# Performance work log

Measured on AMD Instinct MI355X. Metric: run time of the kernel, lower is better.

## Reference

```python
import jax, jax.numpy as jnp
import numpy as np
import math

B, N, C, A, H = 1, 320, 128, 32, 4  # batch, n_res, rep_2d channels, attn channels, heads


def _layernorm(x, w, b, eps=1e-5):
    mu = jnp.mean(x, axis=-1, keepdims=True)
    var = jnp.var(x, axis=-1, keepdims=True)
    return (x - mu) * jax.lax.rsqrt(var + eps) * w + b


def setup_inputs() -> dict:
    key = jax.random.key(0)
    ks = jax.random.split(key, 12)
    s = 0.02
    return {
        "x2d": jax.random.normal(ks[0], (B, N, N, C), dtype=jnp.float32),
        "mask": jnp.ones((B, N, N), dtype=jnp.float32),
        "norm_w": jnp.ones((C,), dtype=jnp.float32),
        "norm_b": jnp.zeros((C,), dtype=jnp.float32),
        "Wq": jax.random.normal(ks[1], (C, A * H), dtype=jnp.float32) * s,
        "Wk": jax.random.normal(ks[2], (C, A * H), dtype=jnp.float32) * s,
        "Wv": jax.random.normal(ks[3], (C, A * H), dtype=jnp.float32) * s,
        "Wb": jax.random.normal(ks[4], (C, H), dtype=jnp.float32) * s,
        "Wg": jax.random.normal(ks[5], (C, A * H), dtype=jnp.float32) * s,
        "bg": jnp.zeros((A * H,), dtype=jnp.float32),
        "Wo": jax.random.normal(ks[6], (A * H, C), dtype=jnp.float32) * s,
        "bo": jnp.zeros((C,), dtype=jnp.float32),
    }


def reference(x2d, mask, norm_w, norm_b, Wq, Wk, Wv, Wb, Wg, bg, Wo, bo):
    xn = _layernorm(x2d, norm_w, norm_b)                      # [B,N,N,C]
    # note: torch .view(..., A, H) splits the output channel as (A, H)
    q = (xn @ Wq).reshape(B, N, N, A, H)
    k = (xn @ Wk).reshape(B, N, N, A, H)
    v = (xn @ Wv).reshape(B, N, N, A, H)
    b = xn @ Wb                                               # [B,N,N,H] -> b[b,j,k,h]
    g = jax.nn.sigmoid((xn @ Wg + bg).reshape(B, N, N, A, H))
    w = jnp.einsum('bijch,bikch->bijkh', q, k) / math.sqrt(A)
    # torch: b.unsqueeze(1).transpose(2,3) => w[b,i,j,k,h] += b[b,k,j,h]
    w = w + jnp.transpose(b, (0, 2, 1, 3))[:, None]           # [B,1,N,N,H]
    w = (w + 100.0) * mask[:, :, None, :, None] - 100.0
    w = jax.nn.softmax(w, axis=-2)                            # over k
    out = jnp.einsum('bijkh,bikch->bijch', w, v) * g          # [B,N,N,A,H]
    out = out.reshape(B, N, N, A * H) @ Wo + bo               # [B,N,N,C]
    out = out * mask[..., None]
    return out
```

## Files before the change

### kernel.cpp

```cpp
#include <hip/hip_runtime.h>
#include <hip/hip_bf16.h>
#include <math.h>

#define N 320
#define C 128
#define A 32
#define H 4
#define NPOS (N*N)

typedef __attribute__((ext_vector_type(8))) __bf16 bf16x8;
typedef __attribute__((ext_vector_type(16))) float f32x16;

union frag_u { int4 i; bf16x8 v; unsigned u[4]; };

#define MFMA32(va, vb, vc) __builtin_amdgcn_mfma_f32_32x32x16_bf16((va), (vb), (vc), 0, 0, 0)

#define WAVE_LDS_FENCE() do { \
    asm volatile("s_waitcnt lgkmcnt(0)" ::: "memory"); \
    __builtin_amdgcn_sched_barrier(0); \
} while (0)

static __device__ __forceinline__ unsigned pk_bf16(float lo, float hi) {
    union { __hip_bfloat162 h; unsigned u; } cv;
    cv.h = __float22bfloat162_rn(make_float2(lo, hi));
    return cv.u;
}

static __device__ __forceinline__ float bf16_to_f32(unsigned short u) {
    union { unsigned u; float f; } c;
    c.u = ((unsigned)u) << 16;
    return c.f;
}

__global__ __launch_bounds__(256)
void wprep_kernel(const float* __restrict__ Wq,
                  const float* __restrict__ Wk,
                  const float* __restrict__ Wv,
                  const float* __restrict__ Wg,
                  const float* __restrict__ Wo,
                  unsigned short* __restrict__ WF) {
    const float isq = 0.17677669529663687f;
    int tid = blockIdx.x * 256 + threadIdx.x;
    int lane = tid & 63;
    int kk = (tid >> 6) & 7;
    int ct = (tid >> 9) & 3;
    int mat = tid >> 11;
    const float* src = (mat == 0) ? Wq : (mat == 1) ? Wk : (mat == 2) ? Wv
                     : (mat == 3) ? Wg : Wo;
    float scl = (mat == 0) ? isq : 1.0f;
    int col = ct * 32 + (lane & 31);
    int c0 = kk * 16 + (lane >> 5) * 8;
    float v[8];
    #pragma unroll
    for (int e = 0; e < 8; e++) {
        int rr = c0 + e;
        int srow = (mat == 4) ? (((rr & 31) << 2) | (rr >> 5)) : rr;
        v[e] = src[(size_t)srow * 128 + col] * scl;
    }
    int4 out;
    out.x = pk_bf16(v[0], v[1]);
    out.y = pk_bf16(v[2], v[3]);
    out.z = pk_bf16(v[4], v[5]);
    out.w = pk_bf16(v[6], v[7]);
    *(int4*)((char*)WF + (size_t)tid * 16) = out;
}

__global__ __launch_bounds__(256)
void btrans_kernel(const float* __restrict__ Bp, float* __restrict__ BpT) {
    __shared__ float tile[64][65];
    const int b = blockIdx.x;
    const int h = b / 25;
    const int bk = (b % 25) / 5;
    const int bj = b % 5;
    const int k0 = bk * 64, j0 = bj * 64;
    const float* src = Bp + (size_t)h * NPOS;
    float* dst = BpT + (size_t)h * NPOS;
    const int t = threadIdx.x;
    #pragma unroll
    for (int u = 0; u < 16; ++u) {
        int idx = u * 256 + t;
        int kk = idx >> 6, jj = idx & 63;
        tile[kk][jj] = src[(size_t)(k0 + kk) * N + j0 + jj];
    }
    __syncthreads();
    #pragma unroll
    for (int u = 0; u < 16; ++u) {
        int idx = u * 256 + t;
        int jj = idx >> 6, kk = idx & 63;
        dst[(size_t)(j0 + jj) * N + k0 + kk] = tile[kk][jj];
    }
}

__global__ __launch_bounds__(256)
void ln_proj_kernel(const float* __restrict__ x2d,
                    const float* __restrict__ norm_w,
                    const float* __restrict__ norm_b,
                    const float* __restrict__ Wb,
                    const float* __restrict__ bg,
                    const unsigned short* __restrict__ WF,
                    unsigned short* __restrict__ Qb,
                    unsigned short* __restrict__ Kb,
                    unsigned short* __restrict__ Vta,
                    unsigned short* __restrict__ Gb,
                    float* __restrict__ Bp) {
    __shared__ __align__(16) unsigned char shbuf[16896];
    unsigned char* xnb = shbuf;

    const int t = threadIdx.x;
    const int gpos0 = blockIdx.x * 32;

    {
        const int r = t >> 3, s = t & 7;
        const float4* src = (const float4*)(x2d + (size_t)(gpos0 + r) * 128 + s * 16);
        float4 xv[4];
        #pragma unroll
        for (int u = 0; u < 4; u++) xv[u] = src[u];
        float sum = 0.f, sq = 0.f;
        #pragma unroll
        for (int u = 0; u < 4; u++) {
            sum += xv[u].x + xv[u].y + xv[u].z + xv[u].w;
            sq += xv[u].x * xv[u].x + xv[u].y * xv[u].y
                + xv[u].z * xv[u].z + xv[u].w * xv[u].w;
        }
        sum += __shfl_xor(sum, 1); sum += __shfl_xor(sum, 2); sum += __shfl_xor(sum, 4);
        sq  += __shfl_xor(sq, 1);  sq  += __shfl_xor(sq, 2);  sq  += __shfl_xor(sq, 4);
        float mean = sum * (1.0f / 128.0f);
        float var  = sq * (1.0f / 128.0f) - mean * mean;
        float rstd = rsqrtf(var + 1e-5f);

        const float4* wsrc = (const float4*)(norm_w + s * 16);
        const float4* bsrc = (const float4*)(norm_b + s * 16);
        const float4* wb4  = (const float4*)Wb;
        float pb0 = 0.f, pb1 = 0.f, pb2 = 0.f, pb3 = 0.f;
        float4 xe;
        #pragma unroll
        for (int u = 0; u < 4; u++) {
            float4 wv = wsrc[u], bv = bsrc[u], x4 = xv[u];
            float4 xn;
            xn.x = (x4.x - mean) * rstd * wv.x + bv.x;
            xn.y = (x4.y - mean) * rstd * wv.y + bv.y;
            xn.z = (x4.z - mean) * rstd * wv.z + bv.z;
            xn.w = (x4.w - mean) * rstd * wv.w + bv.w;
            int cb = s * 16 + u * 4;
            float4 w0 = wb4[cb + 0], w1 = wb4[cb + 1], w2 = wb4[cb + 2], w3 = wb4[cb + 3];
            pb0 = fmaf(xn.x, w0.x, fmaf(xn.y, w1.x, fmaf(xn.z, w2.x, fmaf(xn.w, w3.x, pb0))));
            pb1 = fmaf(xn.x, w0.y, fmaf(xn.y, w1.y, fmaf(xn.z, w2.y, fmaf(xn.w, w3.y, pb1))));
            pb2 = fmaf(xn.x, w0.z, fmaf(xn.y, w1.z, fmaf(xn.z, w2.z, fmaf(xn.w, w3.z, pb2))));
            pb3 = fmaf(xn.x, w0.w, fmaf(xn.y, w1.w, fmaf(xn.z, w2.w, fmaf(xn.w, w3.w, pb3))));
            if (u & 1) {
                int g = s * 2 + (u >> 1);
                int4 gr;
                gr.x = pk_bf16(xe.x, xe.y);
                gr.y = pk_bf16(xe.z, xe.w);
                gr.z = pk_bf16(xn.x, xn.y);
                gr.w = pk_bf16(xn.z, xn.w);
                *(int4*)(xnb + r * 256 + ((g ^ (r & 7)) << 4)) = gr;
            } else {
                xe = xn;
            }
        }
        pb0 += __shfl_xor(pb0, 1); pb0 += __shfl_xor(pb0, 2); pb0 += __shfl_xor(pb0, 4);
        pb1 += __shfl_xor(pb1, 1); pb1 += __shfl_xor(pb1, 2); pb1 += __shfl_xor(pb1, 4);
        pb2 += __shfl_xor(pb2, 1); pb2 += __shfl_xor(pb2, 2); pb2 += __shfl_xor(pb2, 4);
        pb3 += __shfl_xor(pb3, 1); pb3 += __shfl_xor(pb3, 2); pb3 += __shfl_xor(pb3, 4);
        if (s < 4) {
            float pbsel = (s == 0) ? pb0 : (s == 1) ? pb1 : (s == 2) ? pb2 : pb3;
            Bp[(size_t)s * NPOS + gpos0 + r] = pbsel;
        }
    }
    __syncthreads();

    const int lane = t & 63;
    const int w = t >> 6;
    const int col = lane & 31;
    const int hi = lane >> 5;

    frag_u af[8];
    #pragma unroll
    for (int kk = 0; kk < 8; kk++)
        af[kk].i = *(const int4*)(xnb + col * 256 + (((kk * 2 + hi) ^ (col & 7)) << 4));
    __syncthreads();

    const char* wf = (const char*)WF + (size_t)w * 4 * 8 * 1024;
    float* stage_w = (float*)shbuf + w * 1056;

    for (int ct = 0; ct < 4; ct++) {
        f32x16 acc;
        #pragma unroll
        for (int r = 0; r < 16; r++) acc[r] = 0.f;
        #pragma unroll
        for (int kk = 0; kk < 8; kk++) {
            frag_u bf;
            bf.i = *(const int4*)(wf + (ct * 8 + kk) * 1024 + lane * 16);
            acc = MFMA32(af[kk].v, bf.v, acc);
        }
        #pragma unroll
        for (int r = 0; r < 16; r++) {
            int patr = (r & 3) + 8 * (r >> 2) + 4 * hi;
            stage_w[col * 33 + patr] = acc[r];
        }
        WAVE_LDS_FENCE();
        if (w < 2) {
            char* dst = (w == 0) ? (char*)Qb : (char*)Kb;
            #pragma unroll
            for (int h = 0; h < 4; h++) {
                float f[4];
                #pragma unroll
                for (int e = 0; e < 4; e++)
                    f[e] = stage_w[((hi * 4 + e) * 4 + h) * 33 + col];
                uint2 val;
                val.x = pk_bf16(f[0], f[1]);
                val.y = pk_bf16(f[2], f[3]);
                *(uint2*)(dst + ((size_t)(h * 4 + ct) * NPOS + gpos0 + col) * 16 + hi * 8) = val;
            }
        } else if (w == 2) {
            int cc = col, half = hi;
            int plane = (cc & 3) * 32 + ct * 8 + (cc >> 2);
            unsigned pk[8];
            #pragma unroll
            for (int j2 = 0; j2 < 8; j2++)
                pk[j2] = pk_bf16(stage_w[cc * 33 + half * 16 + 2 * j2],
                                 stage_w[cc * 33 + half * 16 + 2 * j2 + 1]);
            int4* dst = (int4*)((char*)Vta + ((size_t)plane * NPOS + gpos0 + half * 16) * 2);
            dst[0] = make_int4(pk[0], pk[1], pk[2], pk[3]);
            dst[1] = make_int4(pk[4], pk[5], pk[6], pk[7]);
        } else {
            #pragma unroll
            for (int h = 0; h < 4; h++) {
                float f[4];
                #pragma unroll
                for (int e = 0; e < 4; e++) {
                    float z = stage_w[((hi * 4 + e) * 4 + h) * 33 + col]
                            + bg[ct * 32 + (hi * 4 + e) * 4 + h];
                    f[e] = 1.0f / (1.0f + __expf(-z));
                }
                uint2 val;
                val.x = pk_bf16(f[0], f[1]);
                val.y = pk_bf16(f[2], f[3]);
                *(uint2*)((char*)Gb + ((size_t)(h * 4 + ct) * NPOS + gpos0 + col) * 16 + hi * 8) = val;
            }
        }
        WAVE_LDS_FENCE();
    }
}

__global__ __launch_bounds__(320, 2)
void attn_kernel(const unsigned short* __restrict__ Qb,
                 const unsigned short* __restrict__ Kb,
                 const unsigned short* __restrict__ Vta,
                 const unsigned short* __restrict__ Gb,
                 const float* __restrict__ BpT,
                 const float* __restrict__ mask,
                 unsigned short* __restrict__ Ob) {
    __shared__ __align__(16) unsigned char smem[40960];
    __shared__ float mparr[320];
    __shared__ float m2arr[320];
    unsigned char* Klds = smem;
    unsigned char* Vlds = smem + 20480;

    const int i = blockIdx.x >> 2;
    const int h = blockIdx.x & 3;
    const int t = threadIdx.x;
    const int lane = t & 63;
    const int w = t >> 6;
    const int col = lane & 31;
    const int hi = lane >> 5;
    const int jt0 = w * 64;

    frag_u qf[2][2];
    const char* qplane = (const char*)Qb + ((size_t)(h * 4) * NPOS + (size_t)i * N) * 16;
    #pragma unroll
    for (int jt = 0; jt < 2; ++jt) {
        int jrow = jt0 + jt * 32 + col;
        #pragma unroll
        for (int cf = 0; cf < 2; ++cf) {
            int g = cf * 2 + hi;
            qf[jt][cf].i = *(const int4*)(qplane + ((size_t)g * NPOS + jrow) * 16);
        }
    }

    const char* kplane = (const char*)Kb + ((size_t)(h * 4) * NPOS + (size_t)i * N) * 16;
    #pragma unroll
    for (int it = 0; it < 4; ++it) {
        int4 val = *(const int4*)(kplane + ((size_t)it * NPOS + t) * 16);
        *(int4*)(Klds + t * 64 + ((it ^ ((t >> 1) & 3)) << 4)) = val;
    }
    const char* vbsrc = (const char*)Vta + ((size_t)h * 32 * NPOS + (size_t)i * N) * 2;
    #pragma unroll
    for (int it = 0; it < 4; ++it) {
        int tt = t + it * 320;
        int a = tt / 40, kg = tt % 40;
        int4 val = *(const int4*)(vbsrc + (size_t)a * NPOS * 2 + kg * 16);
        *(int4*)(Vlds + a * 640 + ((kg ^ (a & 7)) << 4)) = val;
    }
    {
        int kt_ = t >> 5, hi_ = (t >> 4) & 1, r_ = t & 15;
        int k = kt_ * 32 + (r_ & 3) + 8 * (r_ >> 2) + 4 * hi_;
        float m_ = mask[(size_t)i * N + k];
        mparr[t] = m_;
        m2arr[t] = fmaf(100.f, m_, -100.f);
    }
    __syncthreads();

    f32x16 accO[2];
    #pragma unroll
    for (int r = 0; r < 16; ++r) { accO[0][r] = 0.f; accO[1][r] = 0.f; }
    float lsum[2] = { 0.f, 0.f };

    const float* br0 = BpT + (size_t)h * NPOS + (size_t)(jt0 + col) * N + 4 * hi;
    const float* br1 = br0 + (size_t)32 * N;

    float4 b0[4], b1[4];
    #pragma unroll
    for (int q = 0; q < 4; ++q) b0[q] = *(const float4*)(br0 + 8 * q);

#define PROCESS_JT(JT, BB)                                                      \
    {                                                                           \
        f32x16 S;                                                               \
        _Pragma("unroll") for (int r = 0; r < 16; ++r) S[r] = 0.f;              \
        __builtin_amdgcn_s_setprio(1);                                          \
        S = MFMA32(kf0.v, qf[JT][0].v, S);                                      \
        S = MFMA32(kf1.v, qf[JT][1].v, S);                                      \
        __builtin_amdgcn_s_setprio(0);                                          \
        float pe[16];                                                           \
        float l0 = 0.f, l1 = 0.f, l2 = 0.f, l3 = 0.f;                           \
        _Pragma("unroll") for (int q = 0; q < 4; ++q) {                         \
            float sv0 = fmaf(S[4*q+0] + BB[q].x, mk4[q].x, m2v[q].x);           \
            float sv1 = fmaf(S[4*q+1] + BB[q].y, mk4[q].y, m2v[q].y);           \
            float sv2 = fmaf(S[4*q+2] + BB[q].z, mk4[q].z, m2v[q].z);           \
            float sv3 = fmaf(S[4*q+3] + BB[q].w, mk4[q].w, m2v[q].w);           \
            pe[4*q+0] = __expf(sv0); pe[4*q+1] = __expf(sv1);                   \
            pe[4*q+2] = __expf(sv2); pe[4*q+3] = __expf(sv3);                   \
            l0 += pe[4*q+0]; l1 += pe[4*q+1];                                   \
            l2 += pe[4*q+2]; l3 += pe[4*q+3];                                   \
        }                                                                       \
        lsum[JT] += (l0 + l1) + (l2 + l3);                                      \
        unsigned p[8];                                                          \
        _Pragma("unroll") for (int q = 0; q < 8; ++q)                           \
            p[q] = pk_bf16(pe[2 * q], pe[2 * q + 1]);                           \
        unsigned x0 = p[0], y0 = p[2];                                          \
        unsigned x1 = p[1], y1 = p[3];                                          \
        unsigned x2 = p[4], y2 = p[6];                                          \
        unsigned x3 = p[5], y3 = p[7];                                          \
        asm("v_permlane32_swap_b32 %0, %1" : "+v"(x0), "+v"(y0));               \
        asm("v_permlane32_swap_b32 %0, %1" : "+v"(x1), "+v"(y1));               \
        asm("v_permlane32_swap_b32 %0, %1" : "+v"(x2), "+v"(y2));               \
        asm("v_permlane32_swap_b32 %0, %1" : "+v"(x3), "+v"(y3));               \
        frag_u bf0, bf1;                                                        \
        bf0.u[0] = x0; bf0.u[1] = x1; bf0.u[2] = y0; bf0.u[3] = y1;             \
        bf1.u[0] = x2; bf1.u[1] = x3; bf1.u[2] = y2; bf1.u[3] = y3;             \
        __builtin_amdgcn_s_setprio(1);                                          \
        accO[JT] = MFMA32(vf0.v, bf0.v, accO[JT]);                              \
        accO[JT] = MFMA32(vf1.v, bf1.v, accO[JT]);                              \
        __builtin_amdgcn_s_setprio(0);                                          \
    }

    for (int kt = 0; kt < 10; ++kt) {
        const int kbase = kt * 32;
        const int krow = kbase + col;
        frag_u kf0, kf1, vf0, vf1;
        kf0.i = *(const int4*)(Klds + krow * 64 + (((0 + hi) ^ ((krow >> 1) & 3)) << 4));
        kf1.i = *(const int4*)(Klds + krow * 64 + (((2 + hi) ^ ((krow >> 1) & 3)) << 4));
        vf0.i = *(const int4*)(Vlds + col * 640 + (((kt * 4 + 0 + hi) ^ (col & 7)) << 4));
        vf1.i = *(const int4*)(Vlds + col * 640 + (((kt * 4 + 2 + hi) ^ (col & 7)) << 4));

        float4 mk4[4], m2v[4];
        const float* mp  = mparr + kbase + hi * 16;
        const float* m2p = m2arr + kbase + hi * 16;
        #pragma unroll
        for (int q = 0; q < 4; ++q) {
            mk4[q] = *(const float4*)(mp + 4 * q);
            m2v[q] = *(const float4*)(m2p + 4 * q);
        }

        #pragma unroll
        for (int q = 0; q < 4; ++q) b1[q] = *(const float4*)(br1 + kbase + 8 * q);

        PROCESS_JT(0, b0)

        if (kt < 9) {
            #pragma unroll
            for (int q = 0; q < 4; ++q) b0[q] = *(const float4*)(br0 + kbase + 32 + 8 * q);
        }

        PROCESS_JT(1, b1)
    }
#undef PROCESS_JT

    __syncthreads();
    float* st = (float*)(smem + w * 8192);
    const char* gplane = (const char*)Gb + ((size_t)(h * 4) * NPOS + (size_t)i * N) * 16;

    #pragma unroll
    for (int jt = 0; jt < 2; ++jt) {
        float lt = lsum[jt] + __shfl_xor(lsum[jt], 32);
        float inv = 1.0f / lt;
        #pragma unroll
        for (int r = 0; r < 16; ++r) {
            const int a = (r & 3) + 8 * (r >> 2) + 4 * hi;
            st[col * 33 + a] = accO[jt][r] * inv;
        }
        WAVE_LDS_FENCE();
        {
            int jj = lane & 31;
            int ah0 = hi * 16;
            int jrow = jt0 + jt * 32 + jj;
            int4 g0 = *(const int4*)(gplane + ((size_t)(2 * hi + 0) * NPOS + jrow) * 16);
            int4 g1 = *(const int4*)(gplane + ((size_t)(2 * hi + 1) * NPOS + jrow) * 16);
            unsigned gw[8] = { (unsigned)g0.x, (unsigned)g0.y, (unsigned)g0.z, (unsigned)g0.w,
                               (unsigned)g1.x, (unsigned)g1.y, (unsigned)g1.z, (unsigned)g1.w };
            unsigned pk8[8];
            #pragma unroll
            for (int e = 0; e < 8; ++e) {
                float ge0 = bf16_to_f32((unsigned short)(gw[e] & 0xffffu));
                float ge1 = bf16_to_f32((unsigned short)(gw[e] >> 16));
                pk8[e] = pk_bf16(st[jj * 33 + ah0 + 2 * e + 0] * ge0,
                                 st[jj * 33 + ah0 + 2 * e + 1] * ge1);
            }
            char* dst = (char*)Ob + (((size_t)i * N + jrow) * 128 + h * 32 + ah0) * 2;
            *(int4*)dst = make_int4(pk8[0], pk8[1], pk8[2], pk8[3]);
            *(int4*)(dst + 16) = make_int4(pk8[4], pk8[5], pk8[6], pk8[7]);
        }
        WAVE_LDS_FENCE();
    }
}

__global__ __launch_bounds__(256)
void outproj_kernel(const unsigned short* __restrict__ Ob,
                    const unsigned short* __restrict__ WoF,
                    const float* __restrict__ bo,
                    const float* __restrict__ mask,
                    float* __restrict__ out) {
    __shared__ __align__(16) unsigned char obs[64 * 256];
    __shared__ float stage[4][32 * 65];

    const int t = threadIdx.x;
    const int gpos0 = blockIdx.x * 64;

    {
        const int r = t >> 2, s = t & 3;
        const char* src = (const char*)Ob + ((size_t)(gpos0 + r) * 128 + s * 32) * 2;
        #pragma unroll
        for (int u = 0; u < 4; ++u) {
            int4 v = *(const int4*)(src + u * 16);
            int g = s * 4 + u;
            *(int4*)(obs + r * 256 + ((g ^ (r & 7)) << 4)) = v;
        }
    }
    __syncthreads();

    const int lane = t & 63;
    const int w = t >> 6;
    const int col = lane & 31;
    const int hi = lane >> 5;

    f32x16 acc0, acc1;
    float bocol = bo[w * 32 + col];
    #pragma unroll
    for (int r = 0; r < 16; ++r) { acc0[r] = bocol; acc1[r] = bocol; }

    const char* wf = (const char*)WoF + (size_t)w * 8 * 1024;
    #pragma unroll
    for (int kk = 0; kk < 8; ++kk) {
        frag_u bf, a0, a1;
        bf.i = *(const int4*)(wf + kk * 1024 + lane * 16);
        int row0 = col, row1 = 32 + col;
        a0.i = *(const int4*)(obs + row0 * 256 + (((kk * 2 + hi) ^ (row0 & 7)) << 4));
        a1.i = *(const int4*)(obs + row1 * 256 + (((kk * 2 + hi) ^ (row1 & 7)) << 4));
        acc0 = MFMA32(a0.v, bf.v, acc0);
        acc1 = MFMA32(a1.v, bf.v, acc1);
    }

    float* st = stage[w];
    #pragma unroll
    for (int r = 0; r < 16; ++r) {
        int patr = (r & 3) + 8 * (r >> 2) + 4 * hi;
        st[col * 65 + patr] = acc0[r];
        st[col * 65 + 32 + patr] = acc1[r];
    }
    WAVE_LDS_FENCE();
    {
        int row = lane;
        float mv = mask[gpos0 + row];
        float4* dst = (float4*)(out + (size_t)(gpos0 + row) * 128 + w * 32);
        #pragma unroll
        for (int u = 0; u < 8; ++u) {
            float4 o;
            o.x = st[(4 * u + 0) * 65 + row] * mv;
            o.y = st[(4 * u + 1) * 65 + row] * mv;
            o.z = st[(4 * u + 2) * 65 + row] * mv;
            o.w = st[(4 * u + 3) * 65 + row] * mv;
            dst[u] = o;
        }
    }
}

extern "C" void kernel_launch(void* const* d_in, const int* in_sizes, int n_in,
                              void* d_out, int out_size, void* d_ws, size_t ws_size,
                              hipStream_t stream) {
    const float* x2d    = (const float*)d_in[0];
    const float* mask   = (const float*)d_in[1];
    const float* norm_w = (const float*)d_in[2];
    const float* norm_b = (const float*)d_in[3];
    const float* Wq     = (const float*)d_in[4];
    const float* Wk     = (const float*)d_in[5];
    const float* Wv     = (const float*)d_in[6];
    const float* Wb     = (const float*)d_in[7];
    const float* Wg     = (const float*)d_in[8];
    const float* bg     = (const float*)d_in[9];
    const float* Wo     = (const float*)d_in[10];
    const float* bo     = (const float*)d_in[11];
    float* out = (float*)d_out;

    char* ws = (char*)d_ws;
    float* Bp  = (float*)ws;                                   ws += (size_t)H * NPOS * 4;
    float* BpT = (float*)ws;                                   ws += (size_t)H * NPOS * 4;
    unsigned short* Qb  = (unsigned short*)ws;                 ws += (size_t)NPOS * C * 2;
    unsigned short* Kb  = (unsigned short*)ws;                 ws += (size_t)NPOS * C * 2;
    unsigned short* Vta = (unsigned short*)ws;                 ws += (size_t)NPOS * C * 2;
    unsigned short* Gb  = (unsigned short*)ws;                 ws += (size_t)NPOS * C * 2;
    unsigned short* Ob  = (unsigned short*)ws;                 ws += (size_t)NPOS * C * 2;
    unsigned short* WF  = (unsigned short*)ws;
    unsigned short* WoF = WF + (size_t)4 * 16384;

    wprep_kernel<<<40, 256, 0, stream>>>(Wq, Wk, Wv, Wg, Wo, WF);

    ln_proj_kernel<<<NPOS / 32, 256, 0, stream>>>(x2d, norm_w, norm_b, Wb, bg,
                                                  WF, Qb, Kb, Vta, Gb, Bp);

    btrans_kernel<<<H * 25, 256, 0, stream>>>(Bp, BpT);

    attn_kernel<<<N * H, 320, 0, stream>>>(Qb, Kb, Vta, Gb, BpT, mask, Ob);

    outproj_kernel<<<NPOS / 64, 256, 0, stream>>>(Ob, WoF, bo, mask, out);
}
```

Before: 182.3 us.

## Store pair bias as bf16 and stream K fragments from global instead of LDS

The transposed pair-bias tensor is now stored in bf16, which halves its bytes read by the attention kernel, and is widened back to fp32 in registers. K fragments are no longer staged in LDS. Each wave loads them straight from global memory with a one-tile-ahead prefetch. This cuts LDS use from about 40 KB to 21 KB, which may allow more resident blocks. In exchange, K reads are repeated per wave through L2 instead of shared, and the bias loses precision.

```diff
diff --git a/kernel.cpp b/kernel.cpp
--- a/kernel.cpp
+++ b/kernel.cpp
@@ -29,6 +29,12 @@
 static __device__ __forceinline__ float bf16_to_f32(unsigned short u) {
     union { unsigned u; float f; } c;
     c.u = ((unsigned)u) << 16;
+    return c.f;
+}
+
+static __device__ __forceinline__ float u32_as_f32(unsigned u) {
+    union { unsigned u; float f; } c;
+    c.u = u;
     return c.f;
 }
 
@@ -66,7 +72,7 @@
 }
 
 __global__ __launch_bounds__(256)
-void btrans_kernel(const float* __restrict__ Bp, float* __restrict__ BpT) {
+void btrans_kernel(const float* __restrict__ Bp, unsigned short* __restrict__ BpTb) {
     __shared__ float tile[64][65];
     const int b = blockIdx.x;
     const int h = b / 25;
@@ -74,7 +80,7 @@
     const int bj = b % 5;
     const int k0 = bk * 64, j0 = bj * 64;
     const float* src = Bp + (size_t)h * NPOS;
-    float* dst = BpT + (size_t)h * NPOS;
+    unsigned short* dst = BpTb + (size_t)h * NPOS;
     const int t = threadIdx.x;
     #pragma unroll
     for (int u = 0; u < 16; ++u) {
@@ -87,7 +93,8 @@
     for (int u = 0; u < 16; ++u) {
         int idx = u * 256 + t;
         int jj = idx >> 6, kk = idx & 63;
-        dst[(size_t)(j0 + jj) * N + k0 + kk] = tile[kk][jj];
+        dst[(size_t)(j0 + jj) * N + k0 + kk] =
+            (unsigned short)(pk_bf16(tile[kk][jj], 0.f) & 0xffffu);
     }
 }
 
@@ -249,14 +256,12 @@
                  const unsigned short* __restrict__ Kb,
                  const unsigned short* __restrict__ Vta,
                  const unsigned short* __restrict__ Gb,
-                 const float* __restrict__ BpT,
+                 const unsigned short* __restrict__ BpTb,
                  const float* __restrict__ mask,
                  unsigned short* __restrict__ Ob) {
-    __shared__ __align__(16) unsigned char smem[40960];
+    __shared__ __align__(16) unsigned char smem[21120];
     __shared__ float mparr[320];
     __shared__ float m2arr[320];
-    unsigned char* Klds = smem;
-    unsigned char* Vlds = smem + 20480;
 
     const int i = blockIdx.x >> 2;
     const int h = blockIdx.x & 3;
@@ -279,19 +284,15 @@
         }
     }
 
-    const char* kplane = (const char*)Kb + ((size_t)(h * 4) * NPOS + (size_t)i * N) * 16;
-    #pragma unroll
-    for (int it = 0; it < 4; ++it) {
-        int4 val = *(const int4*)(kplane + ((size_t)it * NPOS + t) * 16);
-        *(int4*)(Klds + t * 64 + ((it ^ ((t >> 1) & 3)) << 4)) = val;
-    }
+    const char* kpl = (const char*)Kb + ((size_t)(h * 4) * NPOS + (size_t)i * N) * 16;
+
     const char* vbsrc = (const char*)Vta + ((size_t)h * 32 * NPOS + (size_t)i * N) * 2;
     #pragma unroll
     for (int it = 0; it < 4; ++it) {
         int tt = t + it * 320;
         int a = tt / 40, kg = tt % 40;
         int4 val = *(const int4*)(vbsrc + (size_t)a * NPOS * 2 + kg * 16);
-        *(int4*)(Vlds + a * 640 + ((kg ^ (a & 7)) << 4)) = val;
+        *(int4*)(smem + a * 640 + ((kg ^ (a & 7)) << 4)) = val;
     }
     {
         int kt_ = t >> 5, hi_ = (t >> 4) & 1, r_ = t & 15;
@@ -300,6 +301,9 @@
         mparr[t] = m_;
         m2arr[t] = fmaf(100.f, m_, -100.f);
     }
+    frag_u kf0, kf1, kf0n, kf1n;
+    kf0.i = *(const int4*)(kpl + ((size_t)hi * NPOS + col) * 16);
+    kf1.i = *(const int4*)(kpl + ((size_t)(2 + hi) * NPOS + col) * 16);
     __syncthreads();
 
     f32x16 accO[2];
@@ -307,12 +311,12 @@
     for (int r = 0; r < 16; ++r) { accO[0][r] = 0.f; accO[1][r] = 0.f; }
     float lsum[2] = { 0.f, 0.f };
 
-    const float* br0 = BpT + (size_t)h * NPOS + (size_t)(jt0 + col) * N + 4 * hi;
-    const float* br1 = br0 + (size_t)32 * N;
-
-    float4 b0[4], b1[4];
-    #pragma unroll
-    for (int q = 0; q < 4; ++q) b0[q] = *(const float4*)(br0 + 8 * q);
+    const unsigned short* br0 = BpTb + (size_t)h * NPOS + (size_t)(jt0 + col) * N + 4 * hi;
+    const unsigned short* br1 = br0 + (size_t)32 * N;
+
+    uint2 b0[4], b1[4];
+    #pragma unroll
+    for (int q = 0; q < 4; ++q) b0[q] = *(const uint2*)(br0 + 8 * q);
 
 #define PROCESS_JT(JT, BB)                                                      \
     {                                                                           \
@@ -325,10 +329,14 @@
         float pe[16];                                                           \
         float l0 = 0.f, l1 = 0.f, l2 = 0.f, l3 = 0.f;                           \
         _Pragma("unroll") for (int q = 0; q < 4; ++q) {                         \
-            float sv0 = fmaf(S[4*q+0] + BB[q].x, mk4[q].x, m2v[q].x);           \
-            float sv1 = fmaf(S[4*q+1] + BB[q].y, mk4[q].y, m2v[q].y);           \
-            float sv2 = fmaf(S[4*q+2] + BB[q].z, mk4[q].z, m2v[q].z);           \
-            float sv3 = fmaf(S[4*q+3] + BB[q].w, mk4[q].w, m2v[q].w);           \
+            float bb0 = u32_as_f32(BB[q].x << 16);                              \
+            float bb1 = u32_as_f32(BB[q].x & 0xffff0000u);                      \
+            float bb2 = u32_as_f32(BB[q].y << 16);                              \
+            float bb3 = u32_as_f32(BB[q].y & 0xffff0000u);                      \
+            float sv0 = fmaf(S[4*q+0] + bb0, mk4[q].x, m2v[q].x);               \
+            float sv1 = fmaf(S[4*q+1] + bb1, mk4[q].y, m2v[q].y);               \
+            float sv2 = fmaf(S[4*q+2] + bb2, mk4[q].z, m2v[q].z);               \
+            float sv3 = fmaf(S[4*q+3] + bb3, mk4[q].w, m2v[q].w);               \
             pe[4*q+0] = __expf(sv0); pe[4*q+1] = __expf(sv1);                   \
             pe[4*q+2] = __expf(sv2); pe[4*q+3] = __expf(sv3);                   \
             l0 += pe[4*q+0]; l1 += pe[4*q+1];                                   \
@@ -357,12 +365,15 @@
 
     for (int kt = 0; kt < 10; ++kt) {
         const int kbase = kt * 32;
-        const int krow = kbase + col;
-        frag_u kf0, kf1, vf0, vf1;
-        kf0.i = *(const int4*)(Klds + krow * 64 + (((0 + hi) ^ ((krow >> 1) & 3)) << 4));
-        kf1.i = *(const int4*)(Klds + krow * 64 + (((2 + hi) ^ ((krow >> 1) & 3)) << 4));
-        vf0.i = *(const int4*)(Vlds + col * 640 + (((kt * 4 + 0 + hi) ^ (col & 7)) << 4));
-        vf1.i = *(const int4*)(Vlds + col * 640 + (((kt * 4 + 2 + hi) ^ (col & 7)) << 4));
+        frag_u vf0, vf1;
+        vf0.i = *(const int4*)(smem + col * 640 + (((kt * 4 + 0 + hi) ^ (col & 7)) << 4));
+        vf1.i = *(const int4*)(smem + col * 640 + (((kt * 4 + 2 + hi) ^ (col & 7)) << 4));
+
+        if (kt < 9) {
+            int krn = kbase + 32 + col;
+            kf0n.i = *(const int4*)(kpl + ((size_t)hi * NPOS + krn) * 16);
+            kf1n.i = *(const int4*)(kpl + ((size_t)(2 + hi) * NPOS + krn) * 16);
+        }
 
         float4 mk4[4], m2v[4];
         const float* mp  = mparr + kbase + hi * 16;
@@ -374,21 +385,24 @@
         }
 
         #pragma unroll
-        for (int q = 0; q < 4; ++q) b1[q] = *(const float4*)(br1 + kbase + 8 * q);
+        for (int q = 0; q < 4; ++q) b1[q] = *(const uint2*)(br1 + kbase + 8 * q);
 
         PROCESS_JT(0, b0)
 
         if (kt < 9) {
             #pragma unroll
-            for (int q = 0; q < 4; ++q) b0[q] = *(const float4*)(br0 + kbase + 32 + 8 * q);
+            for (int q = 0; q < 4; ++q) b0[q] = *(const uint2*)(br0 + kbase + 32 + 8 * q);
         }
 
         PROCESS_JT(1, b1)
+
+        kf0 = kf0n;
+        kf1 = kf1n;
     }
 #undef PROCESS_JT
 
     __syncthreads();
-    float* st = (float*)(smem + w * 8192);
+    float* st = (float*)(smem + w * 4224);
     const char* gplane = (const char*)Gb + ((size_t)(h * 4) * NPOS + (size_t)i * N) * 16;
 
     #pragma unroll
@@ -514,7 +528,7 @@
 
     char* ws = (char*)d_ws;
     float* Bp  = (float*)ws;                                   ws += (size_t)H * NPOS * 4;
-    float* BpT = (float*)ws;                                   ws += (size_t)H * NPOS * 4;
+    unsigned short* BpTb = (unsigned short*)ws;                ws += (size_t)H * NPOS * 4;
     unsigned short* Qb  = (unsigned short*)ws;                 ws += (size_t)NPOS * C * 2;
     unsigned short* Kb  = (unsigned short*)ws;                 ws += (size_t)NPOS * C * 2;
     unsigned short* Vta = (unsigned short*)ws;                 ws += (size_t)NPOS * C * 2;
@@ -528,9 +542,9 @@
     ln_proj_kernel<<<NPOS / 32, 256, 0, stream>>>(x2d, norm_w, norm_b, Wb, bg,
                                                   WF, Qb, Kb, Vta, Gb, Bp);
 
-    btrans_kernel<<<H * 25, 256, 0, stream>>>(Bp, BpT);
-
-    attn_kernel<<<N * H, 320, 0, stream>>>(Qb, Kb, Vta, Gb, BpT, mask, Ob);
+    btrans_kernel<<<H * 25, 256, 0, stream>>>(Bp, BpTb);
+
+    attn_kernel<<<N * H, 320, 0, stream>>>(Qb, Kb, Vta, Gb, BpTb, mask, Ob);
 
     outproj_kernel<<<NPOS / 64, 256, 0, stream>>>(Ob, WoF, bo, mask, out);
 }
```

Result: no change. 184.8 us (+1.4%).
